# Performance work log

Measured on AMD Instinct MI355X. Metric: run time of the kernel, lower is better.

Reference implementation:

```python
import jax, jax.numpy as jnp
import numpy as np
from functools import partial

NUM_QUERIES = 900
TOPK_PRE = 100      # topk(100) in source
TOPK_POST = 20      # keep_inds[:20] in source
IOU_THR = 0.7


def cxcywh_to_xyxy(b):
    cx, cy, w, h = b[..., 0], b[..., 1], b[..., 2], b[..., 3]
    return jnp.stack([cx - 0.5 * w, cy - 0.5 * h, cx + 0.5 * w, cy + 0.5 * h], axis=-1)


def nms_single(boxes, scores):
    # boxes: [K,4] xyxy, already sorted by descending score (top_k output).
    # Single class per patch in this module, so batched_nms == plain nms.
    K = boxes.shape[0]
    area = jnp.clip(boxes[:, 2] - boxes[:, 0], 0) * jnp.clip(boxes[:, 3] - boxes[:, 1], 0)
    lt = jnp.maximum(boxes[:, None, :2], boxes[None, :, :2])
    rb = jnp.minimum(boxes[:, None, 2:], boxes[None, :, 2:])
    wh = jnp.clip(rb - lt, 0)
    inter = wh[..., 0] * wh[..., 1]
    iou = inter / (area[:, None] + area[None, :] - inter + 1e-7)  # [K,K]
    idx = jnp.arange(K)

    def body(i, keep):
        sup = (iou[i] > IOU_THR) & (idx > i) & keep[i]
        return keep & (~sup)

    keep = jax.lax.fori_loop(0, K, body, jnp.ones((K,), bool))
    rank = jnp.cumsum(keep) - 1
    valid = keep & (rank < TOPK_POST)
    slot = jnp.where(valid, rank, TOPK_POST)  # invalid entries scatter into dropped slot
    sel_s = jnp.zeros((TOPK_POST + 1,), scores.dtype).at[slot].set(jnp.where(valid, scores, 0.0))[:TOPK_POST]
    sel_b = jnp.zeros((TOPK_POST + 1, 4), boxes.dtype).at[slot].set(jnp.where(valid[:, None], boxes, 0.0))[:TOPK_POST]
    vmask = jnp.zeros((TOPK_POST + 1,), bool).at[slot].set(valid)[:TOPK_POST]
    return sel_s, sel_b, vmask


def setup_inputs() -> dict:
    key = jax.random.key(0)
    k1, k2, k3, k4 = jax.random.split(key, 4)
    BS, P, Q, C = 16, 64, NUM_QUERIES, 2
    pred_logits = jax.random.normal(k1, (BS, 1, P * Q, C), jnp.float32)
    pred_boxes = jax.random.uniform(k2, (BS, 1, P * Q, 4), jnp.float32, minval=0.05, maxval=0.6)
    target_sizes = jax.random.uniform(k3, (BS, 2), jnp.float32, minval=480.0, maxval=1333.0)  # (h, w)
    labels = jax.random.randint(k4, (BS, P), 0, 80, jnp.int32)
    return {"pred_logits": pred_logits, "pred_boxes": pred_boxes,
            "target_sizes": target_sizes, "labels": labels}


def reference(pred_logits, pred_boxes, target_sizes, labels):
    BS = pred_logits.shape[0]
    Q = NUM_QUERIES
    score = jax.nn.sigmoid(pred_logits[:, 0, :, -1])          # [BS, N]
    boxes = cxcywh_to_xyxy(pred_boxes[:, 0])                   # [BS, N, 4]
    img_h, img_w = target_sizes[:, 0], target_sizes[:, 1]
    scale = jnp.stack([img_w, img_h, img_w, img_h], axis=-1)   # [BS, 4]
    boxes = boxes * scale[:, None, :]
    P = score.shape[1] // Q
    score = score.reshape(BS, P, Q)
    boxes = boxes.reshape(BS, P, Q, 4)
    top_s, top_i = jax.lax.top_k(score, TOPK_PRE)              # [BS, P, 100]
    top_b = jnp.take_along_axis(boxes, top_i[..., None], axis=2)  # [BS, P, 100, 4]
    sel_s, sel_b, vmask = jax.vmap(nms_single)(
        top_b.reshape(BS * P, TOPK_PRE, 4), top_s.reshape(BS * P, TOPK_PRE))
    sel_s = sel_s.reshape(BS, P, TOPK_POST)
    sel_b = sel_b.reshape(BS, P, TOPK_POST, 4)
    vmask = vmask.reshape(BS, P, TOPK_POST)
    sel_l = jnp.where(vmask, labels[:, :, None], -1)
    return sel_s, sel_b, sel_l, vmask
```

## Files before the change

### kernel.cpp

```cpp
#include <hip/hip_runtime.h>
#include <stdint.h>

#define NQ 900
#define TOPK_PRE 100
#define TOPK_POST 20
#define IOU_THR 0.7f
#define THREADS 256

typedef unsigned long long u64;

__device__ __forceinline__ u64 umin64(u64 a, u64 b) { return a < b ? a : b; }
__device__ __forceinline__ u64 umax64(u64 a, u64 b) { return a > b ? a : b; }


__global__ __launch_bounds__(THREADS)
void ovnms_kernel(const float* __restrict__ logits,
                  const float* __restrict__ boxes,
                  const float* __restrict__ tsize,
                  const int*   __restrict__ labels,
                  float* __restrict__ out)
{
#pragma clang fp contract(off)
    const int row  = blockIdx.x;
    const int b    = row >> 6;
    const int p    = row & 63;
    const int tid  = threadIdx.x;
    const int lane = tid & 63;
    const int wid  = tid >> 6;

    __shared__ u64 wl[4 * 128];
    __shared__ u64 md[2 * 128];
    __shared__ u64 fin[128];
    __shared__ u64 sup0[TOPK_PRE], sup1[TOPK_PRE];
    __shared__ float x1s[TOPK_PRE], y1s[TOPK_PRE], x2s[TOPK_PRE], y2s[TOPK_PRE];
    __shared__ float areas[TOPK_PRE], scs[TOPK_PRE];
    __shared__ int   slots[TOPK_POST];
    __shared__ int   nkeep;

    const float2* l2 = (const float2*)(logits + ((size_t)b * 57600 + (size_t)p * NQ) * 2);
    u64 kr[4];
#pragma unroll
    for (int r = 0; r < 4; ++r) {
        int q = wid * 64 + lane + r * 256;
        u64 key = ~0ull;
        if (q < NQ) {
            float x = l2[q].y;
            float s = 1.0f / (1.0f + expf(-x));
            unsigned u = __float_as_uint(s);
            key = ((u64)(~u) << 32) | (unsigned)q;
        }
        kr[r] = key;
    }

#pragma unroll
    for (int k = 2; k <= 256; k <<= 1) {
#pragma unroll
        for (int j = k >> 1; j > 0; j >>= 1) {
            if (j >= 64) {
                const int jr = j >> 6;
#pragma unroll
                for (int r = 0; r < 4; ++r) {
                    if ((r & jr) == 0) {
                        const int rp = r | jr;
                        bool up = (((r * 64) & k) == 0);
                        u64 lo = umin64(kr[r], kr[rp]);
                        u64 hi = umax64(kr[r], kr[rp]);
                        kr[r]  = up ? lo : hi;
                        kr[rp] = up ? hi : lo;
                    }
                }
            } else {
#pragma unroll
                for (int r = 0; r < 4; ++r) {
                    bool up = (((r * 64 + lane) & k) == 0);
                    u64 part = __shfl_xor(kr[r], j);
                    bool lower = ((lane & j) == 0);
                    kr[r] = (up == lower) ? umin64(kr[r], part) : umax64(kr[r], part);
                }
            }
        }
    }

    wl[wid * 128 + lane]      = kr[0];
    wl[wid * 128 + 64 + lane] = kr[1];
    __syncthreads();

    if (wid < 2) {
        const u64* A = &wl[(2 * wid) * 128];
        const u64* B = &wl[(2 * wid + 1) * 128];
        u64 c0 = umin64(A[lane],      B[127 - lane]);
        u64 c1 = umin64(A[64 + lane], B[63 - lane]);
        u64 lo = umin64(c0, c1), hi = umax64(c0, c1);
        c0 = lo; c1 = hi;
#pragma unroll
        for (int j = 32; j > 0; j >>= 1) {
            bool lower = (lane & j) == 0;
            u64 p0 = __shfl_xor(c0, j);
            u64 p1 = __shfl_xor(c1, j);
            c0 = lower ? umin64(c0, p0) : umax64(c0, p0);
            c1 = lower ? umin64(c1, p1) : umax64(c1, p1);
        }
        md[wid * 128 + lane]      = c0;
        md[wid * 128 + 64 + lane] = c1;
    }
    __syncthreads();

    if (wid == 0) {
        const u64* A = md;
        const u64* B = md + 128;
        u64 c0 = umin64(A[lane],      B[127 - lane]);
        u64 c1 = umin64(A[64 + lane], B[63 - lane]);
        u64 lo = umin64(c0, c1), hi = umax64(c0, c1);
        c0 = lo; c1 = hi;
#pragma unroll
        for (int j = 32; j > 0; j >>= 1) {
            bool lower = (lane & j) == 0;
            u64 p0 = __shfl_xor(c0, j);
            u64 p1 = __shfl_xor(c1, j);
            c0 = lower ? umin64(c0, p0) : umax64(c0, p0);
            c1 = lower ? umin64(c1, p1) : umax64(c1, p1);
        }
        fin[lane]      = c0;
        fin[64 + lane] = c1;
    }
    __syncthreads();

    if (tid < TOPK_PRE) {
        u64 key = fin[tid];
        int q = (int)(key & 0xFFFFFFFFu);
        scs[tid] = __uint_as_float(~(unsigned)(key >> 32));
        const float* brow = boxes + ((size_t)b * 57600 + (size_t)p * NQ + (size_t)q) * 4;
        float cx = brow[0], cy = brow[1], w = brow[2], h = brow[3];
        float ih = tsize[b * 2 + 0];
        float iw = tsize[b * 2 + 1];
        float xa = (cx - 0.5f * w) * iw;
        float ya = (cy - 0.5f * h) * ih;
        float xb = (cx + 0.5f * w) * iw;
        float yb = (cy + 0.5f * h) * ih;
        x1s[tid] = xa; y1s[tid] = ya; x2s[tid] = xb; y2s[tid] = yb;
        areas[tid] = fmaxf(xb - xa, 0.0f) * fmaxf(yb - ya, 0.0f);
    }
    __syncthreads();

    for (int i = wid; i < TOPK_PRE; i += 4) {
        float xi1 = x1s[i], yi1 = y1s[i], xi2 = x2s[i], yi2 = y2s[i], ai = areas[i];
        int j = lane;
        bool b0 = false;
        if (j < i) {
            float ltx = fmaxf(xi1, x1s[j]);
            float lty = fmaxf(yi1, y1s[j]);
            float rbx = fminf(xi2, x2s[j]);
            float rby = fminf(yi2, y2s[j]);
            float wx = fmaxf(rbx - ltx, 0.0f);
            float wy = fmaxf(rby - lty, 0.0f);
            float inter = wx * wy;
            float iou = inter / (((ai + areas[j]) - inter) + 1e-7f);
            b0 = iou > IOU_THR;
        }
        u64 m0 = __ballot(b0);
        j = 64 + lane;
        bool b1 = false;
        if (j < i) {
            float ltx = fmaxf(xi1, x1s[j]);
            float lty = fmaxf(yi1, y1s[j]);
            float rbx = fminf(xi2, x2s[j]);
            float rby = fminf(yi2, y2s[j]);
            float wx = fmaxf(rbx - ltx, 0.0f);
            float wy = fmaxf(rby - lty, 0.0f);
            float inter = wx * wy;
            float iou = inter / (((ai + areas[j]) - inter) + 1e-7f);
            b1 = iou > IOU_THR;
        }
        u64 m1 = __ballot(b1);
        if (lane == 0) { sup0[i] = m0; sup1[i] = m1; }
    }
    __syncthreads();

    if (tid == 0) {
        u64 kept0 = 0, kept1 = 0;
        int r = 0;
#pragma unroll 10
        for (int i = 0; i < TOPK_PRE; ++i) {
            u64 s0 = sup0[i] & kept0;
            u64 s1 = sup1[i] & kept1;
            if ((s0 | s1) == 0ull) {
                if (i < 64) kept0 |= 1ull << i;
                else        kept1 |= 1ull << (i - 64);
                if (r < TOPK_POST) slots[r] = i;
                r++;
            }
        }
        nkeep = r < TOPK_POST ? r : TOPK_POST;
    }
    __syncthreads();

    if (tid < TOPK_POST) {
        size_t o = (size_t)row * TOPK_POST + (size_t)tid;
        float s = 0.0f, xa = 0.0f, ya = 0.0f, xb = 0.0f, yb = 0.0f;
        float lab = -1.0f, m = 0.0f;
        if (tid < nkeep) {
            int i = slots[tid];
            s = scs[i];
            xa = x1s[i]; ya = y1s[i]; xb = x2s[i]; yb = y2s[i];
            lab = (float)labels[row];
            m = 1.0f;
        }
        out[o] = s;
        float* ob = out + 20480 + o * 4;
        ob[0] = xa; ob[1] = ya; ob[2] = xb; ob[3] = yb;
        out[102400 + o] = lab;
        out[122880 + o] = m;
    }
}

extern "C" void kernel_launch(void* const* d_in, const int* in_sizes, int n_in,
                              void* d_out, int out_size, void* d_ws, size_t ws_size,
                              hipStream_t stream) {
    const float* logits = (const float*)d_in[0];
    const float* boxes  = (const float*)d_in[1];
    const float* tsize  = (const float*)d_in[2];
    const int*   labels = (const int*)d_in[3];
    float* out = (float*)d_out;

    ovnms_kernel<<<dim3(1024), dim3(THREADS), 0, stream>>>(logits, boxes, tsize, labels, out);
}
```

Before: 42.33 us.

## Parallelize NMS suppression scan across a wavefront and cache column boxes in registers

Replaces the single-thread serial suppression scan with a wavefront-wide scan, where each lane tracks the alive status of its candidate boxes and a ballot decides whether box i is kept. The final kept indices are found by bit-selection on the keep masks instead of a shared slot list. The IoU matrix loop now holds each lane's column boxes in registers rather than re-reading them from shared memory every iteration. This is meant to shorten the serial critical path, at the cost of a ballot per step across 100 iterations.

Result: faster. 37.07 us (-12.4%).

```diff
diff --git a/kernel.cpp b/kernel.cpp
--- a/kernel.cpp
+++ b/kernel.cpp
@@ -34,8 +34,7 @@
     __shared__ u64 sup0[TOPK_PRE], sup1[TOPK_PRE];
     __shared__ float x1s[TOPK_PRE], y1s[TOPK_PRE], x2s[TOPK_PRE], y2s[TOPK_PRE];
     __shared__ float areas[TOPK_PRE], scs[TOPK_PRE];
-    __shared__ int   slots[TOPK_POST];
-    __shared__ int   nkeep;
+    __shared__ u64 keep0s, keep1s;
 
     const float2* l2 = (const float2*)(logits + ((size_t)b * 57600 + (size_t)p * NQ) * 2);
     u64 kr[4];
@@ -142,66 +141,103 @@
     }
     __syncthreads();
 
-    for (int i = wid; i < TOPK_PRE; i += 4) {
-        float xi1 = x1s[i], yi1 = y1s[i], xi2 = x2s[i], yi2 = y2s[i], ai = areas[i];
-        int j = lane;
-        bool b0 = false;
-        if (j < i) {
-            float ltx = fmaxf(xi1, x1s[j]);
-            float lty = fmaxf(yi1, y1s[j]);
-            float rbx = fminf(xi2, x2s[j]);
-            float rby = fminf(yi2, y2s[j]);
-            float wx = fmaxf(rbx - ltx, 0.0f);
-            float wy = fmaxf(rby - lty, 0.0f);
-            float inter = wx * wy;
-            float iou = inter / (((ai + areas[j]) - inter) + 1e-7f);
-            b0 = iou > IOU_THR;
-        }
-        u64 m0 = __ballot(b0);
-        j = 64 + lane;
-        bool b1 = false;
-        if (j < i) {
-            float ltx = fmaxf(xi1, x1s[j]);
-            float lty = fmaxf(yi1, y1s[j]);
-            float rbx = fminf(xi2, x2s[j]);
-            float rby = fminf(yi2, y2s[j]);
-            float wx = fmaxf(rbx - ltx, 0.0f);
-            float wy = fmaxf(rby - lty, 0.0f);
-            float inter = wx * wy;
-            float iou = inter / (((ai + areas[j]) - inter) + 1e-7f);
-            b1 = iou > IOU_THR;
-        }
-        u64 m1 = __ballot(b1);
-        if (lane == 0) { sup0[i] = m0; sup1[i] = m1; }
-    }
-    __syncthreads();
-
-    if (tid == 0) {
-        u64 kept0 = 0, kept1 = 0;
-        int r = 0;
-#pragma unroll 10
-        for (int i = 0; i < TOPK_PRE; ++i) {
-            u64 s0 = sup0[i] & kept0;
-            u64 s1 = sup1[i] & kept1;
-            if ((s0 | s1) == 0ull) {
-                if (i < 64) kept0 |= 1ull << i;
-                else        kept1 |= 1ull << (i - 64);
-                if (r < TOPK_POST) slots[r] = i;
-                r++;
-            }
-        }
-        nkeep = r < TOPK_POST ? r : TOPK_POST;
+    {
+        const float xj1a = x1s[lane], yj1a = y1s[lane];
+        const float xj2a = x2s[lane], yj2a = y2s[lane], aja = areas[lane];
+        const int  j2   = lane + 64;
+        const bool hv2  = j2 < TOPK_PRE;
+        const int  j2c  = hv2 ? j2 : 0;
+        const float xj1b = x1s[j2c], yj1b = y1s[j2c];
+        const float xj2b = x2s[j2c], yj2b = y2s[j2c], ajb = areas[j2c];
+
+#pragma unroll 5
+        for (int i = wid; i < TOPK_PRE; i += 4) {
+            float xi1 = x1s[i], yi1 = y1s[i], xi2 = x2s[i], yi2 = y2s[i], ai = areas[i];
+            bool b0 = false;
+            if (lane < i) {
+                float ltx = fmaxf(xi1, xj1a);
+                float lty = fmaxf(yi1, yj1a);
+                float rbx = fminf(xi2, xj2a);
+                float rby = fminf(yi2, yj2a);
+                float wx = fmaxf(rbx - ltx, 0.0f);
+                float wy = fmaxf(rby - lty, 0.0f);
+                float inter = wx * wy;
+                float iou = inter / (((ai + aja) - inter) + 1e-7f);
+                b0 = iou > IOU_THR;
+            }
+            u64 m0 = __ballot(b0);
+            bool b1 = false;
+            if (hv2 && j2 < i) {
+                float ltx = fmaxf(xi1, xj1b);
+                float lty = fmaxf(yi1, yj1b);
+                float rbx = fminf(xi2, xj2b);
+                float rby = fminf(yi2, yj2b);
+                float wx = fmaxf(rbx - ltx, 0.0f);
+                float wy = fmaxf(rby - lty, 0.0f);
+                float inter = wx * wy;
+                float iou = inter / (((ai + ajb) - inter) + 1e-7f);
+                b1 = iou > IOU_THR;
+            }
+            u64 m1 = __ballot(b1);
+            if (lane == 0) { sup0[i] = m0; sup1[i] = m1; }
+        }
+    }
+    __syncthreads();
+
+    if (wid == 0) {
+        u64 r0a = sup0[lane];
+        u64 r1a = sup1[lane];
+        const int  j2  = lane + 64;
+        const bool hv2 = j2 < TOPK_PRE;
+        u64 r0b = hv2 ? sup0[j2] : 0ull;
+        u64 r1b = hv2 ? sup1[j2] : 0ull;
+        bool alive_a = true;
+        bool alive_b = hv2;
+
+#pragma unroll 4
+        for (int i = 0; i < 64; ++i) {
+            u64 bal = __ballot(alive_a);
+            if ((bal >> i) & 1ull) {
+                alive_a = alive_a && !((r0a >> i) & 1ull);
+                alive_b = alive_b && !((r0b >> i) & 1ull);
+            }
+        }
+#pragma unroll 4
+        for (int i = 64; i < TOPK_PRE; ++i) {
+            u64 bal = __ballot(alive_b);
+            if ((bal >> (i - 64)) & 1ull) {
+                alive_a = alive_a && !((r1a >> (i - 64)) & 1ull);
+                alive_b = alive_b && !((r1b >> (i - 64)) & 1ull);
+            }
+        }
+        u64 B0 = __ballot(alive_a);
+        u64 B1 = __ballot(alive_b);
+        if (lane == 0) { keep0s = B0; keep1s = B1; }
     }
     __syncthreads();
 
     if (tid < TOPK_POST) {
+        u64 K0 = keep0s, K1 = keep1s;
+        int c0 = __popcll(K0);
+        int idx = -1;
+        if (tid < c0) {
+            u64 x = K0;
+            for (int k = 0; k < tid; ++k) x &= x - 1;
+            idx = __ffsll(x) - 1;
+        } else {
+            int t = tid - c0;
+            if (t < __popcll(K1)) {
+                u64 x = K1;
+                for (int k = 0; k < t; ++k) x &= x - 1;
+                idx = 64 + __ffsll(x) - 1;
+            }
+        }
         size_t o = (size_t)row * TOPK_POST + (size_t)tid;
         float s = 0.0f, xa = 0.0f, ya = 0.0f, xb = 0.0f, yb = 0.0f;
         float lab = -1.0f, m = 0.0f;
-        if (tid < nkeep) {
-            int i = slots[tid];
-            s = scs[i];
-            xa = x1s[i]; ya = y1s[i]; xb = x2s[i]; yb = y2s[i];
+        if (idx >= 0) {
+            s = scs[idx];
+            xa = x1s[idx]; ya = y1s[idx]; xb = x2s[idx]; yb = y2s[idx];
             lab = (float)labels[row];
             m = 1.0f;
         }
```
